# Kernel optimization log

Measured on AMD Instinct MI355X. Metric: run time of the kernel, lower is better.

The kernel has to match this reference:

```python
import jax, jax.numpy as jnp
import numpy as np

B, S, D, H = 4, 2048, 1024, 16
HD = D // H  # head size = 64
EPS = 0.01


def _col_normalize(x):
    # tf reduce(): (x - mean) / (std + 0.01), mean/std over axis=-2 (sequence axis)
    mean = jnp.mean(x, axis=-2, keepdims=True)
    std = jnp.std(x, axis=-2, keepdims=True)
    return (x - mean) / (std + EPS)


def setup_inputs() -> dict:
    key = jax.random.key(0)
    ks = jax.random.split(key, 8)
    query = jax.random.normal(ks[0], (B, S, D), dtype=jnp.float32)
    value = jax.random.normal(ks[1], (B, S, D), dtype=jnp.float32)
    # causal additive mask: 0 on/below diagonal, -1e9 above
    mask = jnp.where(jnp.tril(jnp.ones((S, S), dtype=bool)), 0.0, -1e9).astype(jnp.float32)
    w_scale = 0.02
    Wq = jax.random.normal(ks[2], (D, D), dtype=jnp.float32) * w_scale
    bq = jnp.zeros((D,), dtype=jnp.float32)
    Wkv = jax.random.normal(ks[3], (D, 2 * D), dtype=jnp.float32) * w_scale
    bkv = jnp.zeros((2 * D,), dtype=jnp.float32)
    Wo = jax.random.normal(ks[4], (D, D), dtype=jnp.float32) * w_scale
    bo = jnp.zeros((D,), dtype=jnp.float32)
    return {"query": query, "value": value, "mask": mask,
            "Wq": Wq, "bq": bq, "Wkv": Wkv, "bkv": bkv, "Wo": Wo, "bo": bo}


def reference(query, value, mask, Wq, bq, Wkv, bkv, Wo, bo):
    scale = 1.0 / jnp.sqrt(jnp.float32(HD))
    q = query @ Wq + bq          # [B,S,D]
    kv = value @ Wkv + bkv       # [B,S,2D]
    # normalize_columns=True: mean/std over sequence axis before head split
    q = _col_normalize(q)
    kv = _col_normalize(kv)
    # split into 2H chunks of HD: first H chunks -> K heads, last H -> V heads
    k = kv[..., :D].reshape(B, S, H, HD)
    v = kv[..., D:].reshape(B, S, H, HD)
    qh = q.reshape(B, S, H, HD)
    score = jnp.einsum('bqhd,bkhd->bhqk', qh, k) * scale + mask  # [B,H,S,S]
    attn = jax.nn.softmax(score, axis=-1)
    heads = jnp.einsum('bhqk,bkhd->bqhd', attn, v).reshape(B, S, D)
    return heads @ Wo + bo
```

## Files before the change

kernel.cpp:

```cpp
#include <hip/hip_runtime.h>
#include <stdint.h>

#define NB 4
#define NS 2048
#define ND 1024
#define NH 16
#define EPSN 0.01f

typedef short bf16x8 __attribute__((ext_vector_type(8)));
typedef float f32x4 __attribute__((ext_vector_type(4)));

__device__ __forceinline__ float bf2f(unsigned short u){
  union { float f; unsigned int i; } x; x.i = ((unsigned int)u) << 16; return x.f;
}
__device__ __forceinline__ unsigned short f2bf(float f){
  union { float f; unsigned int i; } x; x.f = f;
  unsigned int r = x.i + 0x7FFFu + ((x.i >> 16) & 1u);
  return (unsigned short)(r >> 16);
}

#define MFMA16(a,b,c) __builtin_amdgcn_mfma_f32_16x16x32_bf16(a,b,c,0,0,0)

__device__ __forceinline__ void gload_lds16(const void* g, void* l){
  __builtin_amdgcn_global_load_lds(
    (const __attribute__((address_space(1))) unsigned int*)g,
    (__attribute__((address_space(3))) unsigned int*)l, 16, 0, 0);
}

__global__ __launch_bounds__(256) void k_cvt(const float4* __restrict__ in,
                                             ushort4* __restrict__ out){
  int i = blockIdx.x*256 + threadIdx.x;
  float4 v = in[i];
  ushort4 o;
  o.x = f2bf(v.x); o.y = f2bf(v.y); o.z = f2bf(v.z); o.w = f2bf(v.w);
  out[i] = o;
}

__global__ __launch_bounds__(256) void k_wtrans(const float* __restrict__ W,
                                                unsigned short* __restrict__ Wt,
                                                int K, int N){
  __shared__ float t[64][65];
  int n0 = blockIdx.x*64, k0 = blockIdx.y*64;
  int tid = threadIdx.x;
  int cr = tid & 63, rr = tid >> 6;
  #pragma unroll
  for (int i=0;i<16;++i){
    int r = i*4 + rr;
    t[cr][r] = W[(size_t)(k0 + r)*N + n0 + cr];
  }
  __syncthreads();
  int n = tid >> 2, kc = (tid & 3)*16;
  __align__(16) unsigned short tmp[16];
  #pragma unroll
  for (int j=0;j<16;++j) tmp[j] = f2bf(t[n][kc+j]);
  uint4* dst = reinterpret_cast<uint4*>(&Wt[(size_t)(n0+n)*K + k0 + kc]);
  dst[0] = *reinterpret_cast<uint4*>(&tmp[0]);
  dst[1] = *reinterpret_cast<uint4*>(&tmp[8]);
}

template<int OUTF32>
__global__ __launch_bounds__(256) void k_gemm(const unsigned short* __restrict__ A,
                                              const unsigned short* __restrict__ Bt,
                                              void* __restrict__ Cv,
                                              const float* __restrict__ bias,
                                              int N, int K){
  __shared__ __align__(16) unsigned short As[128*64];
  __shared__ __align__(16) unsigned short Bs[128*64];
  const int tid = threadIdx.x;
  const int w = tid >> 6, l = tid & 63;
  const int m0 = blockIdx.y*128, n0 = blockIdx.x*128;
  const int wr = (w >> 1)*64, wc = (w & 1)*64;
  const int lr8 = l >> 3;
  const int lcs = ((l & 7) ^ lr8)*8;
  const int lane_r = l & 15, lane_g = l >> 4;
  f32x4 acc[4][4] = {};
  for (int kt = 0; kt < K; kt += 64){
    #pragma unroll
    for (int i=0;i<4;++i){
      int seg = w*4 + i;
      int row = seg*8 + lr8;
      gload_lds16(&A[(size_t)(m0+row)*K + kt + lcs], &As[seg*512]);
      gload_lds16(&Bt[(size_t)(n0+row)*K + kt + lcs], &Bs[seg*512]);
    }
    __syncthreads();
    #pragma unroll
    for (int kk=0;kk<2;++kk){
      bf16x8 af[4], bfr[4];
      #pragma unroll
      for (int mt=0;mt<4;++mt){
        int row = wr + mt*16 + lane_r;
        int off = row*128 + kk*64 + lane_g*16;
        off ^= (row & 7) << 4;
        af[mt] = *reinterpret_cast<const bf16x8*>((const char*)As + off);
      }
      #pragma unroll
      for (int nt=0;nt<4;++nt){
        int row = wc + nt*16 + lane_r;
        int off = row*128 + kk*64 + lane_g*16;
        off ^= (row & 7) << 4;
        bfr[nt] = *reinterpret_cast<const bf16x8*>((const char*)Bs + off);
      }
      #pragma unroll
      for (int mt=0;mt<4;++mt)
        #pragma unroll
        for (int nt=0;nt<4;++nt)
          acc[mt][nt] = MFMA16(af[mt], bfr[nt], acc[mt][nt]);
    }
    __syncthreads();
  }
  #pragma unroll
  for (int mt=0;mt<4;++mt)
    #pragma unroll
    for (int nt=0;nt<4;++nt){
      int gn = n0 + wc + nt*16 + lane_r;
      #pragma unroll
      for (int r=0;r<4;++r){
        int gm = m0 + wr + mt*16 + lane_g*4 + r;
        float v = acc[mt][nt][r];
        if (OUTF32)
          ((float*)Cv)[(size_t)gm*N + gn] = v + bias[gn];
        else
          ((unsigned short*)Cv)[(size_t)gm*N + gn] = f2bf(v);
      }
    }
}

__global__ __launch_bounds__(256) void k_colstats(const unsigned short* __restrict__ X,
                                                  float* __restrict__ stats,
                                                  int rowW, int statoff){
  int c = blockIdx.x*512 + threadIdx.x*2;
  int b = blockIdx.z;
  int r0 = blockIdx.y*128;
  const unsigned short* p = X + (size_t)(b*NS + r0)*rowW + c;
  float s0=0.f,s1=0.f,q0=0.f,q1=0.f;
  for (int r=0;r<128;++r){
    unsigned int v = *reinterpret_cast<const unsigned int*>(p);
    float x0 = bf2f((unsigned short)(v & 0xffffu));
    float x1 = bf2f((unsigned short)(v >> 16));
    s0 += x0; q0 += x0*x0; s1 += x1; q1 += x1*x1;
    p += rowW;
  }
  float* sp = stats + (size_t)(b*3*ND + statoff + c)*2;
  atomicAdd(sp+0, s0); atomicAdd(sp+1, q0);
  atomicAdd(sp+2, s1); atomicAdd(sp+3, q1);
}

__global__ __launch_bounds__(256) void k_statsfinal(const float* __restrict__ stats,
                                                    float2* __restrict__ sf){
  int i = blockIdx.x*256 + threadIdx.x;
  float sum = stats[i*2], sq = stats[i*2+1];
  float mean = sum * (1.0f/NS);
  float var = fmaxf(sq * (1.0f/NS) - mean*mean, 0.0f);
  float inv = 1.0f / (sqrtf(var) + EPSN);
  int col = i % (3*ND);
  if (col < ND) inv *= 0.125f * 1.44269504088896340736f;
  sf[i] = make_float2(inv, -mean*inv);
}

__global__ __launch_bounds__(256) void k_norm(unsigned short* __restrict__ X,
                                              const float2* __restrict__ sf,
                                              int rowW, int statoff){
  int idx = blockIdx.x*256 + threadIdx.x;
  int row = idx >> 8;
  int c = (idx & 255)*4;
  int b = row >> 11;
  unsigned short* p = X + (size_t)row*rowW + c;
  uint2 v = *reinterpret_cast<const uint2*>(p);
  const float2* s = sf + (size_t)b*3*ND + statoff + c;
  float2 s0=s[0], s1=s[1], s2=s[2], s3=s[3];
  unsigned int lo = (unsigned int)f2bf(bf2f((unsigned short)(v.x & 0xffffu))*s0.x + s0.y)
                  | ((unsigned int)f2bf(bf2f((unsigned short)(v.x >> 16))*s1.x + s1.y) << 16);
  unsigned int hi = (unsigned int)f2bf(bf2f((unsigned short)(v.y & 0xffffu))*s2.x + s2.y)
                  | ((unsigned int)f2bf(bf2f((unsigned short)(v.y >> 16))*s3.x + s3.y) << 16);
  *reinterpret_cast<uint2*>(p) = make_uint2(lo, hi);
}

__global__ __launch_bounds__(256) void k_vtrans(const unsigned short* __restrict__ kv,
                                                unsigned short* __restrict__ vt,
                                                const float2* __restrict__ sf){
  __shared__ unsigned short t[64][72];
  int s0 = blockIdx.x*64, h = blockIdx.y, b = blockIdx.z;
  int tid = threadIdx.x;
  int rr = tid >> 4;
  int cc = (tid & 15)*4;
  const float2* sp = sf + (size_t)b*3*ND + 2*ND + h*64 + cc;
  float2 f0=sp[0], f1=sp[1], f2v=sp[2], f3=sp[3];
  #pragma unroll
  for (int i=0;i<4;++i){
    int r = i*16 + rr;
    const unsigned short* p = kv + (size_t)(b*NS + s0 + r)*2048 + ND + h*64 + cc;
    uint2 v = *reinterpret_cast<const uint2*>(p);
    t[cc+0][r] = f2bf(bf2f((unsigned short)(v.x & 0xffffu))*f0.x + f0.y);
    t[cc+1][r] = f2bf(bf2f((unsigned short)(v.x >> 16))*f1.x + f1.y);
    t[cc+2][r] = f2bf(bf2f((unsigned short)(v.y & 0xffffu))*f2v.x + f2v.y);
    t[cc+3][r] = f2bf(bf2f((unsigned short)(v.y >> 16))*f3.x + f3.y);
  }
  __syncthreads();
  int hd = tid >> 2, scn = (tid & 3)*16;
  __align__(16) unsigned short tmp[16];
  #pragma unroll
  for (int j=0;j<16;++j) tmp[j] = t[hd][scn+j];
  uint4* dst = reinterpret_cast<uint4*>(&vt[((size_t)(b*NH + h)*64 + hd)*NS + s0 + scn]);
  dst[0] = *reinterpret_cast<uint4*>(&tmp[0]);
  dst[1] = *reinterpret_cast<uint4*>(&tmp[8]);
}

__global__ __launch_bounds__(256) void k_attn(const unsigned short* __restrict__ qn,
                                              const unsigned short* __restrict__ kn,
                                              const unsigned short* __restrict__ vt,
                                              unsigned short* __restrict__ heads){
  __shared__ __align__(16) unsigned short plds[4][32][72];
  const int bid = blockIdx.x;
  const int nb = (bid & 7)*128 + (bid >> 3);
  const int qb = ((nb & 15) + ((nb >> 4) & 3)) & 15;
  const int hb = nb >> 4;
  const int h = hb & 15, b = hb >> 4;
  const int tid = threadIdx.x, w = tid >> 6, l = tid & 63;
  const int lr = l & 15, lg = l >> 4;
  const int q0 = qb*128 + w*32;

  const unsigned short* qp = qn + (size_t)(b*NS + q0 + lr)*ND + h*64 + lg*8;
  bf16x8 qa[2][2];
  qa[0][0] = *reinterpret_cast<const bf16x8*>(qp);
  qa[0][1] = *reinterpret_cast<const bf16x8*>(qp + 32);
  qa[1][0] = *reinterpret_cast<const bf16x8*>(qp + 16*ND);
  qa[1][1] = *reinterpret_cast<const bf16x8*>(qp + 16*ND + 32);

  f32x4 o[2][4] = {};
  float rs0 = 0.f, rs1 = 0.f;
  const unsigned short* kbase = kn + (size_t)b*NS*2048 + h*64 + lg*8;
  const unsigned short* vbase = vt + ((size_t)(b*NH + h)*64 + lr)*NS + lg*8;
  const int ktw = ((q0 + 31) >> 6) + 1;

  for (int kt = 0; kt < ktw; ++kt){
    const int k0 = kt*64;
    bf16x8 kb[4][2];
    #pragma unroll
    for (int kc=0;kc<4;++kc){
      const unsigned short* kp = kbase + (size_t)(k0 + kc*16 + lr)*2048;
      kb[kc][0] = *reinterpret_cast<const bf16x8*>(kp);
      kb[kc][1] = *reinterpret_cast<const bf16x8*>(kp + 32);
    }
    const bool nomask = (k0 + 63 <= q0);
    #pragma unroll
    for (int g=0; g<2; ++g){
      f32x4 sc[4];
      #pragma unroll
      for (int kc=0;kc<4;++kc){
        f32x4 a = {};
        a = MFMA16(kb[kc][0], qa[g][0], a);
        a = MFMA16(kb[kc][1], qa[g][1], a);
        sc[kc] = a;
      }
      const int qrow = q0 + g*16 + lr;
      float acc = 0.f;
      if (nomask){
        #pragma unroll
        for (int kc=0;kc<4;++kc)
          #pragma unroll
          for (int r=0;r<4;++r){
            float pv = exp2f(sc[kc][r]);
            sc[kc][r] = pv;
            acc += pv;
          }
      } else {
        #pragma unroll
        for (int kc=0;kc<4;++kc)
          #pragma unroll
          for (int r=0;r<4;++r){
            int kcol = k0 + kc*16 + lg*4 + r;
            float pv = (kcol <= qrow) ? exp2f(sc[kc][r]) : 0.f;
            sc[kc][r] = pv;
            acc += pv;
          }
      }
      if (g) rs1 += acc; else rs0 += acc;
      #pragma unroll
      for (int kc=0;kc<4;++kc){
        ushort4 pk;
        pk.x = f2bf(sc[kc][0]); pk.y = f2bf(sc[kc][1]);
        pk.z = f2bf(sc[kc][2]); pk.w = f2bf(sc[kc][3]);
        *reinterpret_cast<ushort4*>(&plds[w][g*16 + lr][kc*16 + lg*4]) = pk;
      }
    }
    asm volatile("s_waitcnt lgkmcnt(0)" ::: "memory");
    __builtin_amdgcn_sched_barrier(0);
    bf16x8 pf[2][2];
    #pragma unroll
    for (int g=0; g<2; ++g){
      pf[g][0] = *reinterpret_cast<const bf16x8*>(&plds[w][g*16 + lr][lg*8]);
      pf[g][1] = *reinterpret_cast<const bf16x8*>(&plds[w][g*16 + lr][32 + lg*8]);
    }
    #pragma unroll
    for (int dt=0; dt<4; ++dt){
      const unsigned short* vp = vbase + (size_t)dt*16*NS + k0;
      bf16x8 vb0 = *reinterpret_cast<const bf16x8*>(vp);
      bf16x8 vb1 = *reinterpret_cast<const bf16x8*>(vp + 32);
      o[0][dt] = MFMA16(vb0, pf[0][0], o[0][dt]);
      o[0][dt] = MFMA16(vb1, pf[0][1], o[0][dt]);
      o[1][dt] = MFMA16(vb0, pf[1][0], o[1][dt]);
      o[1][dt] = MFMA16(vb1, pf[1][1], o[1][dt]);
    }
  }

  rs0 += __shfl_xor(rs0, 16, 64); rs0 += __shfl_xor(rs0, 32, 64);
  rs1 += __shfl_xor(rs1, 16, 64); rs1 += __shfl_xor(rs1, 32, 64);
  float inv0 = 1.0f / rs0, inv1 = 1.0f / rs1;
  #pragma unroll
  for (int g=0; g<2; ++g){
    float inv = g ? inv1 : inv0;
    #pragma unroll
    for (int dt=0; dt<4; ++dt){
      ushort4 ov;
      ov.x = f2bf(o[g][dt][0]*inv); ov.y = f2bf(o[g][dt][1]*inv);
      ov.z = f2bf(o[g][dt][2]*inv); ov.w = f2bf(o[g][dt][3]*inv);
      *reinterpret_cast<ushort4*>(
        &heads[(size_t)(b*NS + q0 + g*16 + lr)*ND + h*64 + dt*16 + lg*4]) = ov;
    }
  }
}

extern "C" void kernel_launch(void* const* d_in, const int* in_sizes, int n_in,
                              void* d_out, int out_size, void* d_ws, size_t ws_size,
                              hipStream_t stream){
  (void)in_sizes; (void)n_in; (void)out_size; (void)ws_size;
  const float* query = (const float*)d_in[0];
  const float* value = (const float*)d_in[1];
  const float* Wq  = (const float*)d_in[3];
  const float* Wkv = (const float*)d_in[5];
  const float* Wo  = (const float*)d_in[7];
  const float* bo  = (const float*)d_in[8];

  char* ws = (char*)d_ws;
  unsigned short* qx    = (unsigned short*)(ws + 0);
  unsigned short* vx    = (unsigned short*)(ws + 16777216);
  unsigned short* wqt   = (unsigned short*)(ws + 33554432);
  unsigned short* wkvt  = (unsigned short*)(ws + 35651584);
  unsigned short* wot   = (unsigned short*)(ws + 39845888);
  unsigned short* qbuf  = (unsigned short*)(ws + 41943040);
  unsigned short* kvbuf = (unsigned short*)(ws + 58720256);
  float*          stats = (float*)(ws + 92274688);
  float2*         sfin  = (float2*)(ws + 92372992);
  unsigned short* vtb   = qx;
  unsigned short* heads = vx;

  hipMemsetAsync(stats, 0, NB*3*ND*2*sizeof(float), stream);
  k_cvt<<<8192, 256, 0, stream>>>((const float4*)query, (ushort4*)qx);
  k_cvt<<<8192, 256, 0, stream>>>((const float4*)value, (ushort4*)vx);
  k_wtrans<<<dim3(16,16), 256, 0, stream>>>(Wq, wqt, 1024, 1024);
  k_wtrans<<<dim3(32,16), 256, 0, stream>>>(Wkv, wkvt, 1024, 2048);
  k_wtrans<<<dim3(16,16), 256, 0, stream>>>(Wo, wot, 1024, 1024);
  k_gemm<0><<<dim3(8,64), 256, 0, stream>>>(qx, wqt, qbuf, nullptr, 1024, 1024);
  k_gemm<0><<<dim3(16,64), 256, 0, stream>>>(vx, wkvt, kvbuf, nullptr, 2048, 1024);
  k_colstats<<<dim3(2,16,4), 256, 0, stream>>>(qbuf, stats, 1024, 0);
  k_colstats<<<dim3(4,16,4), 256, 0, stream>>>(kvbuf, stats, 2048, 1024);
  k_statsfinal<<<48, 256, 0, stream>>>(stats, sfin);
  k_norm<<<8192, 256, 0, stream>>>(qbuf, sfin, 1024, 0);
  k_norm<<<8192, 256, 0, stream>>>(kvbuf, sfin, 2048, 1024);
  k_vtrans<<<dim3(32,16,4), 256, 0, stream>>>(kvbuf, vtb, sfin);
  k_attn<<<1024, 256, 0, stream>>>(qbuf, kvbuf, vtb, heads);
  k_gemm<1><<<dim3(8,64), 256, 0, stream>>>(heads, wot, d_out, bo, 1024, 1024);
}
```

Before: 460.3 us.

## Fold K normalization into Q scale, pair causal tiles, use packed bf16 converts

Skips normalizing K separately. The K column scale is folded into the Q scale factor. The K mean shift is dropped because it adds a per-row constant to the scores, which softmax cancels. The attention kernel now gives each wave two query tiles, i and 63-i, which share K/V loads, balancing causal work across 512 blocks. Bf16 conversion switches to the hardware v_cvt_pk_bf16_f32 instruction, and exp2f uses the builtin. This raises register pressure and relies on the softmax being shift-invariant, with no max subtraction, which changes numerics slightly.

```diff
diff --git a/kernel.cpp b/kernel.cpp
--- a/kernel.cpp
+++ b/kernel.cpp
@@ -17,6 +17,11 @@
   union { float f; unsigned int i; } x; x.f = f;
   unsigned int r = x.i + 0x7FFFu + ((x.i >> 16) & 1u);
   return (unsigned short)(r >> 16);
+}
+__device__ __forceinline__ unsigned int cvtpk(float a, float b){
+  unsigned int r;
+  asm("v_cvt_pk_bf16_f32 %0, %1, %2" : "=v"(r) : "v"(a), "v"(b));
+  return r;
 }
 
 #define MFMA16(a,b,c) __builtin_amdgcn_mfma_f32_16x16x32_bf16(a,b,c,0,0,0)
@@ -147,14 +152,21 @@
 
 __global__ __launch_bounds__(256) void k_statsfinal(const float* __restrict__ stats,
                                                     float2* __restrict__ sf){
-  int i = blockIdx.x*256 + threadIdx.x;
-  float sum = stats[i*2], sq = stats[i*2+1];
-  float mean = sum * (1.0f/NS);
-  float var = fmaxf(sq * (1.0f/NS) - mean*mean, 0.0f);
-  float inv = 1.0f / (sqrtf(var) + EPSN);
-  int col = i % (3*ND);
-  if (col < ND) inv *= 0.125f * 1.44269504088896340736f;
-  sf[i] = make_float2(inv, -mean*inv);
+  int t = blockIdx.x*256 + threadIdx.x;
+  int b = t >> 10, c = t & 1023;
+  const float* sb = stats + (size_t)b*3*ND*2;
+  float qs = sb[c*2], qq = sb[c*2+1];
+  float ks = sb[(ND+c)*2], kq = sb[(ND+c)*2+1];
+  float vs = sb[(2*ND+c)*2], vq = sb[(2*ND+c)*2+1];
+  float mq = qs*(1.0f/NS);
+  float invq = 1.0f/(sqrtf(fmaxf(qq*(1.0f/NS)-mq*mq, 0.0f)) + EPSN);
+  float mk = ks*(1.0f/NS);
+  float invk = 1.0f/(sqrtf(fmaxf(kq*(1.0f/NS)-mk*mk, 0.0f)) + EPSN);
+  float mv = vs*(1.0f/NS);
+  float invv = 1.0f/(sqrtf(fmaxf(vq*(1.0f/NS)-mv*mv, 0.0f)) + EPSN);
+  float s = invq*invk*0.125f*1.44269504088896340736f;
+  sf[(size_t)b*3*ND + c] = make_float2(s, -mq*s);
+  sf[(size_t)b*3*ND + 2*ND + c] = make_float2(invv, -mv*invv);
 }
 
 __global__ __launch_bounds__(256) void k_norm(unsigned short* __restrict__ X,
@@ -205,34 +217,89 @@
   dst[1] = *reinterpret_cast<uint4*>(&tmp[8]);
 }
 
+__device__ __forceinline__ void qk_phase(const bf16x8 (&kb)[4][2],
+                                         const bf16x8 (&qa)[2][2],
+                                         float (&rs)[2],
+                                         unsigned short* pl,
+                                         int k0, int q0, int lr, int lg,
+                                         bool masked){
+  #pragma unroll
+  for (int g=0; g<2; ++g){
+    f32x4 sc[4];
+    #pragma unroll
+    for (int kc=0;kc<4;++kc){
+      f32x4 a = {};
+      a = MFMA16(kb[kc][0], qa[g][0], a);
+      a = MFMA16(kb[kc][1], qa[g][1], a);
+      sc[kc] = a;
+    }
+    const int qrow = q0 + g*16 + lr;
+    float acc = 0.f;
+    if (!masked){
+      #pragma unroll
+      for (int kc=0;kc<4;++kc)
+        #pragma unroll
+        for (int r=0;r<4;++r){
+          float pv = __builtin_amdgcn_exp2f(sc[kc][r]);
+          sc[kc][r] = pv; acc += pv;
+        }
+    } else {
+      #pragma unroll
+      for (int kc=0;kc<4;++kc)
+        #pragma unroll
+        for (int r=0;r<4;++r){
+          int kcol = k0 + kc*16 + lg*4 + r;
+          float pv = (kcol <= qrow) ? __builtin_amdgcn_exp2f(sc[kc][r]) : 0.f;
+          sc[kc][r] = pv; acc += pv;
+        }
+    }
+    rs[g] += acc;
+    #pragma unroll
+    for (int kc=0;kc<4;++kc){
+      uint2 pk;
+      pk.x = cvtpk(sc[kc][0], sc[kc][1]);
+      pk.y = cvtpk(sc[kc][2], sc[kc][3]);
+      *reinterpret_cast<uint2*>(pl + (g*16+lr)*72 + kc*16 + lg*4) = pk;
+    }
+  }
+}
+
 __global__ __launch_bounds__(256) void k_attn(const unsigned short* __restrict__ qn,
                                               const unsigned short* __restrict__ kn,
                                               const unsigned short* __restrict__ vt,
                                               unsigned short* __restrict__ heads){
-  __shared__ __align__(16) unsigned short plds[4][32][72];
+  __shared__ __align__(16) unsigned short plds[4][2][32][72];
   const int bid = blockIdx.x;
-  const int nb = (bid & 7)*128 + (bid >> 3);
-  const int qb = ((nb & 15) + ((nb >> 4) & 3)) & 15;
-  const int hb = nb >> 4;
-  const int h = hb & 15, b = hb >> 4;
+  const int xcd = bid & 7, j = bid >> 3;
+  const int bh = xcd*8 + (j & 7);
+  const int p = j >> 3;
+  const int h = bh & 15, b = bh >> 4;
   const int tid = threadIdx.x, w = tid >> 6, l = tid & 63;
   const int lr = l & 15, lg = l >> 4;
-  const int q0 = qb*128 + w*32;
-
-  const unsigned short* qp = qn + (size_t)(b*NS + q0 + lr)*ND + h*64 + lg*8;
-  bf16x8 qa[2][2];
-  qa[0][0] = *reinterpret_cast<const bf16x8*>(qp);
-  qa[0][1] = *reinterpret_cast<const bf16x8*>(qp + 32);
-  qa[1][0] = *reinterpret_cast<const bf16x8*>(qp + 16*ND);
-  qa[1][1] = *reinterpret_cast<const bf16x8*>(qp + 16*ND + 32);
-
-  f32x4 o[2][4] = {};
-  float rs0 = 0.f, rs1 = 0.f;
+  const int i = p*4 + w;
+  const int q0A = i*32, q0B = (63-i)*32;
+  const int ktwA = (i >> 1) + 1, ktwB = ((63-i) >> 1) + 1;
+
+  const unsigned short* qpA = qn + (size_t)(b*NS + q0A + lr)*ND + h*64 + lg*8;
+  const unsigned short* qpB = qn + (size_t)(b*NS + q0B + lr)*ND + h*64 + lg*8;
+  bf16x8 qaA[2][2], qaB[2][2];
+  qaA[0][0] = *reinterpret_cast<const bf16x8*>(qpA);
+  qaA[0][1] = *reinterpret_cast<const bf16x8*>(qpA + 32);
+  qaA[1][0] = *reinterpret_cast<const bf16x8*>(qpA + 16*ND);
+  qaA[1][1] = *reinterpret_cast<const bf16x8*>(qpA + 16*ND + 32);
+  qaB[0][0] = *reinterpret_cast<const bf16x8*>(qpB);
+  qaB[0][1] = *reinterpret_cast<const bf16x8*>(qpB + 32);
+  qaB[1][0] = *reinterpret_cast<const bf16x8*>(qpB + 16*ND);
+  qaB[1][1] = *reinterpret_cast<const bf16x8*>(qpB + 16*ND + 32);
+
+  f32x4 oA[2][4] = {}, oB[2][4] = {};
+  float rsA[2] = {0.f, 0.f}, rsB[2] = {0.f, 0.f};
   const unsigned short* kbase = kn + (size_t)b*NS*2048 + h*64 + lg*8;
   const unsigned short* vbase = vt + ((size_t)(b*NH + h)*64 + lr)*NS + lg*8;
-  const int ktw = ((q0 + 31) >> 6) + 1;
-
-  for (int kt = 0; kt < ktw; ++kt){
+  unsigned short* plA = &plds[w][0][0][0];
+  unsigned short* plB = &plds[w][1][0][0];
+
+  for (int kt = 0; kt < ktwB; ++kt){
     const int k0 = kt*64;
     bf16x8 kb[4][2];
     #pragma unroll
@@ -241,81 +308,67 @@
       kb[kc][0] = *reinterpret_cast<const bf16x8*>(kp);
       kb[kc][1] = *reinterpret_cast<const bf16x8*>(kp + 32);
     }
-    const bool nomask = (k0 + 63 <= q0);
-    #pragma unroll
-    for (int g=0; g<2; ++g){
-      f32x4 sc[4];
-      #pragma unroll
-      for (int kc=0;kc<4;++kc){
-        f32x4 a = {};
-        a = MFMA16(kb[kc][0], qa[g][0], a);
-        a = MFMA16(kb[kc][1], qa[g][1], a);
-        sc[kc] = a;
-      }
-      const int qrow = q0 + g*16 + lr;
-      float acc = 0.f;
-      if (nomask){
-        #pragma unroll
-        for (int kc=0;kc<4;++kc)
-          #pragma unroll
-          for (int r=0;r<4;++r){
-            float pv = exp2f(sc[kc][r]);
-            sc[kc][r] = pv;
-            acc += pv;
-          }
-      } else {
-        #pragma unroll
-        for (int kc=0;kc<4;++kc)
-          #pragma unroll
-          for (int r=0;r<4;++r){
-            int kcol = k0 + kc*16 + lg*4 + r;
-            float pv = (kcol <= qrow) ? exp2f(sc[kc][r]) : 0.f;
-            sc[kc][r] = pv;
-            acc += pv;
-          }
-      }
-      if (g) rs1 += acc; else rs0 += acc;
-      #pragma unroll
-      for (int kc=0;kc<4;++kc){
-        ushort4 pk;
-        pk.x = f2bf(sc[kc][0]); pk.y = f2bf(sc[kc][1]);
-        pk.z = f2bf(sc[kc][2]); pk.w = f2bf(sc[kc][3]);
-        *reinterpret_cast<ushort4*>(&plds[w][g*16 + lr][kc*16 + lg*4]) = pk;
-      }
+    const bool actA = (kt < ktwA);
+    qk_phase(kb, qaB, rsB, plB, k0, q0B, lr, lg, kt == ktwB-1);
+    if (actA) qk_phase(kb, qaA, rsA, plA, k0, q0A, lr, lg, kt == ktwA-1);
+    bf16x8 vb[4][2];
+    #pragma unroll
+    for (int dt=0;dt<4;++dt){
+      const unsigned short* vp = vbase + (size_t)dt*16*NS + k0;
+      vb[dt][0] = *reinterpret_cast<const bf16x8*>(vp);
+      vb[dt][1] = *reinterpret_cast<const bf16x8*>(vp + 32);
     }
     asm volatile("s_waitcnt lgkmcnt(0)" ::: "memory");
     __builtin_amdgcn_sched_barrier(0);
-    bf16x8 pf[2][2];
+    bf16x8 pfB[2][2];
     #pragma unroll
     for (int g=0; g<2; ++g){
-      pf[g][0] = *reinterpret_cast<const bf16x8*>(&plds[w][g*16 + lr][lg*8]);
-      pf[g][1] = *reinterpret_cast<const bf16x8*>(&plds[w][g*16 + lr][32 + lg*8]);
+      pfB[g][0] = *reinterpret_cast<const bf16x8*>(plB + (g*16+lr)*72 + lg*8);
+      pfB[g][1] = *reinterpret_cast<const bf16x8*>(plB + (g*16+lr)*72 + 32 + lg*8);
     }
     #pragma unroll
     for (int dt=0; dt<4; ++dt){
-      const unsigned short* vp = vbase + (size_t)dt*16*NS + k0;
-      bf16x8 vb0 = *reinterpret_cast<const bf16x8*>(vp);
-      bf16x8 vb1 = *reinterpret_cast<const bf16x8*>(vp + 32);
-      o[0][dt] = MFMA16(vb0, pf[0][0], o[0][dt]);
-      o[0][dt] = MFMA16(vb1, pf[0][1], o[0][dt]);
-      o[1][dt] = MFMA16(vb0, pf[1][0], o[1][dt]);
-      o[1][dt] = MFMA16(vb1, pf[1][1], o[1][dt]);
-    }
-  }
-
-  rs0 += __shfl_xor(rs0, 16, 64); rs0 += __shfl_xor(rs0, 32, 64);
-  rs1 += __shfl_xor(rs1, 16, 64); rs1 += __shfl_xor(rs1, 32, 64);
-  float inv0 = 1.0f / rs0, inv1 = 1.0f / rs1;
+      oB[0][dt] = MFMA16(vb[dt][0], pfB[0][0], oB[0][dt]);
+      oB[0][dt] = MFMA16(vb[dt][1], pfB[0][1], oB[0][dt]);
+      oB[1][dt] = MFMA16(vb[dt][0], pfB[1][0], oB[1][dt]);
+      oB[1][dt] = MFMA16(vb[dt][1], pfB[1][1], oB[1][dt]);
+    }
+    if (actA){
+      bf16x8 pfA[2][2];
+      #pragma unroll
+      for (int g=0; g<2; ++g){
+        pfA[g][0] = *reinterpret_cast<const bf16x8*>(plA + (g*16+lr)*72 + lg*8);
+        pfA[g][1] = *reinterpret_cast<const bf16x8*>(plA + (g*16+lr)*72 + 32 + lg*8);
+      }
+      #pragma unroll
+      for (int dt=0; dt<4; ++dt){
+        oA[0][dt] = MFMA16(vb[dt][0], pfA[0][0], oA[0][dt]);
+        oA[0][dt] = MFMA16(vb[dt][1], pfA[0][1], oA[0][dt]);
+        oA[1][dt] = MFMA16(vb[dt][0], pfA[1][0], oA[1][dt]);
+        oA[1][dt] = MFMA16(vb[dt][1], pfA[1][1], oA[1][dt]);
+      }
+    }
+  }
+
   #pragma unroll
   for (int g=0; g<2; ++g){
-    float inv = g ? inv1 : inv0;
+    rsA[g] += __shfl_xor(rsA[g], 16, 64); rsA[g] += __shfl_xor(rsA[g], 32, 64);
+    rsB[g] += __shfl_xor(rsB[g], 16, 64); rsB[g] += __shfl_xor(rsB[g], 32, 64);
+  }
+  #pragma unroll
+  for (int g=0; g<2; ++g){
+    float invA = 1.0f/rsA[g], invB = 1.0f/rsB[g];
     #pragma unroll
     for (int dt=0; dt<4; ++dt){
-      ushort4 ov;
-      ov.x = f2bf(o[g][dt][0]*inv); ov.y = f2bf(o[g][dt][1]*inv);
-      ov.z = f2bf(o[g][dt][2]*inv); ov.w = f2bf(o[g][dt][3]*inv);
-      *reinterpret_cast<ushort4*>(
-        &heads[(size_t)(b*NS + q0 + g*16 + lr)*ND + h*64 + dt*16 + lg*4]) = ov;
+      uint2 ovA, ovB;
+      ovA.x = cvtpk(oA[g][dt][0]*invA, oA[g][dt][1]*invA);
+      ovA.y = cvtpk(oA[g][dt][2]*invA, oA[g][dt][3]*invA);
+      ovB.x = cvtpk(oB[g][dt][0]*invB, oB[g][dt][1]*invB);
+      ovB.y = cvtpk(oB[g][dt][2]*invB, oB[g][dt][3]*invB);
+      *reinterpret_cast<uint2*>(
+        &heads[(size_t)(b*NS + q0A + g*16 + lr)*ND + h*64 + dt*16 + lg*4]) = ovA;
+      *reinterpret_cast<uint2*>(
+        &heads[(size_t)(b*NS + q0B + g*16 + lr)*ND + h*64 + dt*16 + lg*4]) = ovB;
     }
   }
 }
@@ -354,10 +407,9 @@
   k_gemm<0><<<dim3(16,64), 256, 0, stream>>>(vx, wkvt, kvbuf, nullptr, 2048, 1024);
   k_colstats<<<dim3(2,16,4), 256, 0, stream>>>(qbuf, stats, 1024, 0);
   k_colstats<<<dim3(4,16,4), 256, 0, stream>>>(kvbuf, stats, 2048, 1024);
-  k_statsfinal<<<48, 256, 0, stream>>>(stats, sfin);
+  k_statsfinal<<<16, 256, 0, stream>>>(stats, sfin);
   k_norm<<<8192, 256, 0, stream>>>(qbuf, sfin, 1024, 0);
-  k_norm<<<8192, 256, 0, stream>>>(kvbuf, sfin, 2048, 1024);
   k_vtrans<<<dim3(32,16,4), 256, 0, stream>>>(kvbuf, vtb, sfin);
-  k_attn<<<1024, 256, 0, stream>>>(qbuf, kvbuf, vtb, heads);
+  k_attn<<<512, 256, 0, stream>>>(qbuf, kvbuf, vtb, heads);
   k_gemm<1><<<dim3(8,64), 256, 0, stream>>>(heads, wot, d_out, bo, 1024, 1024);
 }
```

Result: faster. 383.0 us (-16.8%).
